# Kernel tuning notes

Measured on AMD Instinct MI355X. Metric: run time of the kernel, lower is better.

Reference implementation:

```python
import jax, jax.numpy as jnp
import numpy as np

B, H, P, L = 8, 512, 512, 2048
HIGH_STAB, LOW_STAB = 0.9, 0.99  # 0 <= high < |lambda| <= low <= 1 (discrete dynamics)


def setup_inputs() -> dict:
    key = jax.random.key(0)
    k_u, k_mag, k_ph, k_b, k_c, k_d = jax.random.split(key, 6)
    u = jax.random.normal(k_u, (B, H, L), dtype=jnp.float32)
    # Frozen diagonal reservoir state matrix Lambda_bar: complex eigenvalues with
    # magnitude in (high_stability, low_stability], random phase (stored as real/imag pairs).
    mag = jax.random.uniform(k_mag, (P,), minval=HIGH_STAB, maxval=LOW_STAB)
    phase = jax.random.uniform(k_ph, (P,), minval=0.0, maxval=2.0 * np.pi)
    Lambda_bar_ri = jnp.stack([mag * jnp.cos(phase), mag * jnp.sin(phase)], axis=-1)  # (P,2)
    B_bar_ri = jax.random.normal(k_b, (P, H, 2), dtype=jnp.float32)  # complex B_bar as real pairs
    C_ri = jax.random.normal(k_c, (H, P, 2), dtype=jnp.float32)      # complex C as real pairs
    D = jax.random.normal(k_d, (H, H), dtype=jnp.float32)
    return {"u": u, "Lambda_bar_ri": Lambda_bar_ri, "B_bar_ri": B_bar_ri, "C_ri": C_ri, "D": D}


def _binary_op(e_i, e_j):
    A_i, Bu_i = e_i
    A_j, Bu_j = e_j
    return (A_j * A_i, A_j * Bu_i + Bu_j)


def reference(u, Lambda_bar_ri, B_bar_ri, C_ri, D):
    Lam = jax.lax.complex(Lambda_bar_ri[:, 0], Lambda_bar_ri[:, 1])        # (P,)
    B_bar = jax.lax.complex(B_bar_ri[..., 0], B_bar_ri[..., 1])            # (P,H)
    C = jax.lax.complex(C_ri[..., 0], C_ri[..., 1])                        # (H,P)
    # Bu_t = B_bar @ u_t for all t, batched: (B,P,L) complex
    Bu = jnp.einsum('ph,bhl->bpl', B_bar, u.astype(B_bar.dtype))
    A = jnp.broadcast_to(Lam[None, :, None], Bu.shape)                     # (B,P,L)
    # Parallel associative scan: x_t = Lam * x_{t-1} + Bu_t
    _, x = jax.lax.associative_scan(_binary_op, (A, Bu), axis=2)           # (B,P,L)
    C_A_Bu = jnp.einsum('hp,bpl->bhl', C, x).real                          # (B,H,L)
    # torch.einsum('hh,bhl->bhl', D, u) uses only the diagonal of D
    Du = jnp.diagonal(D)[None, :, None] * u
    return jax.nn.gelu(C_A_Bu + Du, approximate=False)
```

## Files before the change

kernel.cpp:

```cpp
#include <hip/hip_runtime.h>
#include <cstdint>
#include <cstddef>

#define BB 8
#define HH 512
#define PP 512
#define LL 2048

typedef __attribute__((ext_vector_type(8))) __bf16 bf16x8;
typedef __attribute__((ext_vector_type(4))) float f32x4;

__device__ __forceinline__ uint16_t f2bf(float f) {
  uint32_t u = __builtin_bit_cast(uint32_t, f);
  u += 0x7FFFu + ((u >> 16) & 1u);
  return (uint16_t)(u >> 16);
}

__device__ __forceinline__ void async_copy16(const void* gptr, void* ldsptr) {
  __builtin_amdgcn_global_load_lds(
      (const __attribute__((address_space(1))) unsigned int*)gptr,
      (__attribute__((address_space(3))) unsigned int*)ldsptr,
      16, 0, 0);
}

__global__ __launch_bounds__(256) void prep_mats(
    const float* __restrict__ Bbar, const float* __restrict__ Cri,
    const float* __restrict__ Dm,
    uint16_t* __restrict__ A1, uint16_t* __restrict__ A2,
    float* __restrict__ Dd) {
  int idx = blockIdx.x * 256 + threadIdx.x;
  int p = idx >> 9, h = idx & 511;
  A1[(size_t)p * 512 + h]          = f2bf(Bbar[((size_t)p * 512 + h) * 2 + 0]);
  A1[(size_t)(512 + p) * 512 + h]  = f2bf(Bbar[((size_t)p * 512 + h) * 2 + 1]);
  int h2 = idx >> 9, p2 = idx & 511;
  A2[(size_t)h2 * 1024 + p2]        = f2bf( Cri[((size_t)h2 * 512 + p2) * 2 + 0]);
  A2[(size_t)h2 * 1024 + 512 + p2]  = f2bf(-Cri[((size_t)h2 * 512 + p2) * 2 + 1]);
  if (idx < 512) Dd[idx] = Dm[(size_t)idx * 512 + idx];
}

__global__ __launch_bounds__(256) void scan_kernel(
    const float* __restrict__ Lam, uint16_t* __restrict__ Bu) {
  const int gt = blockIdx.x * 256 + threadIdx.x;
  const int wave = gt >> 6, lane = gt & 63;
  const int b = wave >> 9, p = wave & 511;
  const float lr = Lam[p * 2 + 0], li = Lam[p * 2 + 1];
  float ar = lr, ai = li;
#pragma unroll
  for (int s = 0; s < 5; ++s) { float nr = ar * ar - ai * ai, ni = 2.f * ar * ai; ar = nr; ai = ni; }

  uint16_t* rowre = Bu + ((size_t)(b * 1024 + p)) * 2048 + lane * 32;
  uint16_t* rowim = Bu + ((size_t)(b * 1024 + 512 + p)) * 2048 + lane * 32;
  uint4 vr[4], vi[4];
#pragma unroll
  for (int q = 0; q < 4; ++q) { vr[q] = ((const uint4*)rowre)[q]; vi[q] = ((const uint4*)rowim)[q]; }

  float xr[32], xi[32];
  float sr = 0.f, si = 0.f;
#pragma unroll
  for (int q = 0; q < 4; ++q) {
    uint32_t wr[4] = {vr[q].x, vr[q].y, vr[q].z, vr[q].w};
    uint32_t wi[4] = {vi[q].x, vi[q].y, vi[q].z, vi[q].w};
#pragma unroll
    for (int d = 0; d < 4; ++d) {
      float br0 = __builtin_bit_cast(float, wr[d] << 16);
      float bi0 = __builtin_bit_cast(float, wi[d] << 16);
      float br1 = __builtin_bit_cast(float, wr[d] & 0xFFFF0000u);
      float bi1 = __builtin_bit_cast(float, wi[d] & 0xFFFF0000u);
      int j = q * 8 + d * 2;
      float nr = lr * sr - li * si + br0, ni = lr * si + li * sr + bi0;
      sr = nr; si = ni; xr[j] = sr; xi[j] = si;
      nr = lr * sr - li * si + br1; ni = lr * si + li * sr + bi1;
      sr = nr; si = ni; xr[j + 1] = sr; xi[j + 1] = si;
    }
  }
  float Ar = ar, Ai = ai, Sr = sr, Si = si;
#pragma unroll
  for (int off = 1; off < 64; off <<= 1) {
    float pAr = __shfl_up(Ar, off), pAi = __shfl_up(Ai, off);
    float pSr = __shfl_up(Sr, off), pSi = __shfl_up(Si, off);
    if (lane >= off) {
      float tSr = Ar * pSr - Ai * pSi + Sr;
      float tSi = Ar * pSi + Ai * pSr + Si;
      float tAr = Ar * pAr - Ai * pAi;
      float tAi = Ar * pAi + Ai * pAr;
      Sr = tSr; Si = tSi; Ar = tAr; Ai = tAi;
    }
  }
  float Cr = __shfl_up(Sr, 1), Ci = __shfl_up(Si, 1);
  if (lane == 0) { Cr = 0.f; Ci = 0.f; }
  float fr_ = lr * Cr - li * Ci, fi_ = lr * Ci + li * Cr;
#pragma unroll
  for (int j = 0; j < 32; ++j) {
    xr[j] += fr_; xi[j] += fi_;
    float nfr = fr_ * lr - fi_ * li, nfi = fr_ * li + fi_ * lr;
    fr_ = nfr; fi_ = nfi;
  }
#pragma unroll
  for (int q = 0; q < 4; ++q) {
    uint32_t wr[4], wi[4];
#pragma unroll
    for (int d = 0; d < 4; ++d) {
      int j = q * 8 + d * 2;
      wr[d] = (uint32_t)f2bf(xr[j]) | ((uint32_t)f2bf(xr[j + 1]) << 16);
      wi[d] = (uint32_t)f2bf(xi[j]) | ((uint32_t)f2bf(xi[j + 1]) << 16);
    }
    ((uint4*)rowre)[q] = make_uint4(wr[0], wr[1], wr[2], wr[3]);
    ((uint4*)rowim)[q] = make_uint4(wi[0], wi[1], wi[2], wi[3]);
  }
}

__global__ __launch_bounds__(256) void gemm1_fused(
    const uint16_t* __restrict__ A, const float* __restrict__ U,
    uint16_t* __restrict__ Bu) {
  __shared__ __align__(16) uint16_t Alds[2][128 * 32];
  __shared__ __align__(16) uint16_t Blds[2][128 * 40];
  const int t = threadIdx.x, lane = t & 63, w = t >> 6;
  const int m0 = blockIdx.y * 128, n0 = blockIdx.x * 128, b = blockIdx.z;

  const int ra = t >> 2;
  const int qa = ((t & 3) ^ ((ra >> 1) & 3)) * 8;
  const uint16_t* gA0 = A + (size_t)(m0 + ra) * 512 + qa;
  const uint16_t* gA1 = A + (size_t)(m0 + 64 + ra) * 512 + qa;

  const int kp = t >> 4, lg = t & 15;
  const float* gB = U + ((size_t)b * 512 + 2 * kp) * 2048 + n0 + lg * 8;
  const int bcol = ((kp >> 2) ^ (lg & 3)) * 8 + (kp & 3) * 2;

  f32x4 acc[4][4];
#pragma unroll
  for (int i = 0; i < 4; ++i)
#pragma unroll
    for (int j = 0; j < 4; ++j) acc[i][j] = (f32x4){0.f, 0.f, 0.f, 0.f};

  const int wm = (w >> 1) * 64, wn = (w & 1) * 64;
  const int fr = lane & 15, fq = lane >> 4;
  const int aswz = (fq ^ ((fr >> 1) & 3)) * 8;

  float4 pb0, pb1, pb2, pb3;
  async_copy16(gA0, &Alds[0][t * 8]);
  async_copy16(gA1, &Alds[0][2048 + t * 8]);
  pb0 = *(const float4*)(gB);
  pb1 = *(const float4*)(gB + 4);
  pb2 = *(const float4*)(gB + 2048);
  pb3 = *(const float4*)(gB + 2052);
  {
    float r0[8] = {pb0.x, pb0.y, pb0.z, pb0.w, pb1.x, pb1.y, pb1.z, pb1.w};
    float r1[8] = {pb2.x, pb2.y, pb2.z, pb2.w, pb3.x, pb3.y, pb3.z, pb3.w};
#pragma unroll
    for (int j = 0; j < 8; ++j)
      *(uint32_t*)&Blds[0][(lg * 8 + j) * 40 + bcol] =
          (uint32_t)f2bf(r0[j]) | ((uint32_t)f2bf(r1[j]) << 16);
  }
  __syncthreads();

#pragma unroll 2
  for (int it = 0; it < 16; ++it) {
    const int cur = it & 1, nxt = cur ^ 1;
    const bool pre = (it < 15);
    if (pre) {
      const int kb = (it + 1) * 32;
      async_copy16(gA0 + kb, &Alds[nxt][t * 8]);
      async_copy16(gA1 + kb, &Alds[nxt][2048 + t * 8]);
      const float* s0 = gB + (size_t)kb * 2048;
      pb0 = *(const float4*)(s0);
      pb1 = *(const float4*)(s0 + 4);
      pb2 = *(const float4*)(s0 + 2048);
      pb3 = *(const float4*)(s0 + 2052);
    }
    bf16x8 af[4], bfr[4];
#pragma unroll
    for (int i = 0; i < 4; ++i)
      af[i] = *(const bf16x8*)&Alds[cur][(wm + i * 16 + fr) * 32 + aswz];
#pragma unroll
    for (int j = 0; j < 4; ++j) {
      int n = wn + j * 16 + fr;
      bfr[j] = *(const bf16x8*)&Blds[cur][n * 40 + ((fq ^ ((n >> 3) & 3)) * 8)];
    }
#pragma unroll
    for (int i = 0; i < 4; ++i)
#pragma unroll
      for (int j = 0; j < 4; ++j)
        acc[i][j] = __builtin_amdgcn_mfma_f32_16x16x32_bf16(af[i], bfr[j], acc[i][j], 0, 0, 0);
    if (pre) {
      float r0[8] = {pb0.x, pb0.y, pb0.z, pb0.w, pb1.x, pb1.y, pb1.z, pb1.w};
      float r1[8] = {pb2.x, pb2.y, pb2.z, pb2.w, pb3.x, pb3.y, pb3.z, pb3.w};
#pragma unroll
      for (int j = 0; j < 8; ++j)
        *(uint32_t*)&Blds[nxt][(lg * 8 + j) * 40 + bcol] =
            (uint32_t)f2bf(r0[j]) | ((uint32_t)f2bf(r1[j]) << 16);
      __syncthreads();
    }
  }

  uint16_t* O = Bu + ((size_t)b * 1024 + m0) * 2048 + n0;
#pragma unroll
  for (int i = 0; i < 4; ++i)
#pragma unroll
    for (int j = 0; j < 4; ++j)
#pragma unroll
      for (int r = 0; r < 4; ++r) {
        int mm = wm + i * 16 + fq * 4 + r;
        int nn = wn + j * 16 + fr;
        O[(size_t)mm * 2048 + nn] = f2bf(acc[i][j][r]);
      }
}

__global__ __launch_bounds__(256) void gemm2_fused(
    const uint16_t* __restrict__ A, const uint16_t* __restrict__ X,
    float* __restrict__ Out, const float* __restrict__ Dd,
    const float* __restrict__ Uu) {
  __shared__ __align__(16) uint16_t Alds[2][128 * 32];
  __shared__ __align__(16) uint16_t Blds[2][128 * 40];
  const int t = threadIdx.x, lane = t & 63, w = t >> 6;
  const int m0 = blockIdx.y * 128, n0 = blockIdx.x * 128, b = blockIdx.z;

  const int ra = t >> 2;
  const int qa = ((t & 3) ^ ((ra >> 1) & 3)) * 8;
  const uint16_t* gA0 = A + (size_t)(m0 + ra) * 1024 + qa;
  const uint16_t* gA1 = A + (size_t)(m0 + 64 + ra) * 1024 + qa;

  const int kp = t >> 4, lg = t & 15;
  const uint16_t* gB = X + ((size_t)b * 1024 + 2 * kp) * 2048 + n0 + lg * 8;
  const int bcol = ((kp >> 2) ^ (lg & 3)) * 8 + (kp & 3) * 2;

  f32x4 acc[4][4];
#pragma unroll
  for (int i = 0; i < 4; ++i)
#pragma unroll
    for (int j = 0; j < 4; ++j) acc[i][j] = (f32x4){0.f, 0.f, 0.f, 0.f};

  const int wm = (w >> 1) * 64, wn = (w & 1) * 64;
  const int fr = lane & 15, fq = lane >> 4;
  const int aswz = (fq ^ ((fr >> 1) & 3)) * 8;

  uint4 q0, q1;
  async_copy16(gA0, &Alds[0][t * 8]);
  async_copy16(gA1, &Alds[0][2048 + t * 8]);
  q0 = *(const uint4*)(gB);
  q1 = *(const uint4*)(gB + 2048);
  {
    uint32_t u0[4] = {q0.x, q0.y, q0.z, q0.w};
    uint32_t u1[4] = {q1.x, q1.y, q1.z, q1.w};
#pragma unroll
    for (int d = 0; d < 4; ++d) {
      *(uint32_t*)&Blds[0][(lg * 8 + 2 * d + 0) * 40 + bcol] = (u0[d] & 0xFFFFu) | (u1[d] << 16);
      *(uint32_t*)&Blds[0][(lg * 8 + 2 * d + 1) * 40 + bcol] = (u0[d] >> 16) | (u1[d] & 0xFFFF0000u);
    }
  }
  __syncthreads();

#pragma unroll 2
  for (int it = 0; it < 32; ++it) {
    const int cur = it & 1, nxt = cur ^ 1;
    const bool pre = (it < 31);
    if (pre) {
      const int kb = (it + 1) * 32;
      async_copy16(gA0 + kb, &Alds[nxt][t * 8]);
      async_copy16(gA1 + kb, &Alds[nxt][2048 + t * 8]);
      const uint16_t* s0 = gB + (size_t)kb * 2048;
      q0 = *(const uint4*)(s0);
      q1 = *(const uint4*)(s0 + 2048);
    }
    bf16x8 af[4], bfr[4];
#pragma unroll
    for (int i = 0; i < 4; ++i)
      af[i] = *(const bf16x8*)&Alds[cur][(wm + i * 16 + fr) * 32 + aswz];
#pragma unroll
    for (int j = 0; j < 4; ++j) {
      int n = wn + j * 16 + fr;
      bfr[j] = *(const bf16x8*)&Blds[cur][n * 40 + ((fq ^ ((n >> 3) & 3)) * 8)];
    }
#pragma unroll
    for (int i = 0; i < 4; ++i)
#pragma unroll
      for (int j = 0; j < 4; ++j)
        acc[i][j] = __builtin_amdgcn_mfma_f32_16x16x32_bf16(af[i], bfr[j], acc[i][j], 0, 0, 0);
    if (pre) {
      uint32_t u0[4] = {q0.x, q0.y, q0.z, q0.w};
      uint32_t u1[4] = {q1.x, q1.y, q1.z, q1.w};
#pragma unroll
      for (int d = 0; d < 4; ++d) {
        *(uint32_t*)&Blds[nxt][(lg * 8 + 2 * d + 0) * 40 + bcol] = (u0[d] & 0xFFFFu) | (u1[d] << 16);
        *(uint32_t*)&Blds[nxt][(lg * 8 + 2 * d + 1) * 40 + bcol] = (u0[d] >> 16) | (u1[d] & 0xFFFF0000u);
      }
      __syncthreads();
    }
  }

  const size_t base = ((size_t)b * 512 + m0) * 2048 + n0;
  float* O = Out + base;
  const float* Ub = Uu + base;
#pragma unroll
  for (int i = 0; i < 4; ++i)
#pragma unroll
    for (int r = 0; r < 4; ++r) {
      int mm = wm + i * 16 + fq * 4 + r;
      float dv = Dd[m0 + mm];
#pragma unroll
      for (int j = 0; j < 4; ++j) {
        int nn = wn + j * 16 + fr;
        float xv = acc[i][j][r] + dv * Ub[(size_t)mm * 2048 + nn];
        O[(size_t)mm * 2048 + nn] = 0.5f * xv * (1.f + erff(xv * 0.70710678118654752f));
      }
    }
}

extern "C" void kernel_launch(void* const* d_in, const int* in_sizes, int n_in,
                              void* d_out, int out_size, void* d_ws, size_t ws_size,
                              hipStream_t stream) {
  const float* u    = (const float*)d_in[0];
  const float* Lam  = (const float*)d_in[1];
  const float* Bbar = (const float*)d_in[2];
  const float* Cri  = (const float*)d_in[3];
  const float* Dm   = (const float*)d_in[4];
  float* out = (float*)d_out;

  char* ws = (char*)d_ws;
  uint16_t* Bu = (uint16_t*)(ws);
  uint16_t* A1 = (uint16_t*)(ws + 33554432);
  uint16_t* A2 = (uint16_t*)(ws + 34603008);
  float*    Dd = (float*)   (ws + 35651584);

  prep_mats<<<1024, 256, 0, stream>>>(Bbar, Cri, Dm, A1, A2, Dd);
  gemm1_fused<<<dim3(16, 8, BB), 256, 0, stream>>>(A1, u, Bu);
  scan_kernel<<<1024, 256, 0, stream>>>(Lam, Bu);
  gemm2_fused<<<dim3(16, 4, BB), 256, 0, stream>>>(A2, Bu, out, Dd, u);
}
```

Baseline: 193.0 us.

## Load GEMM A fragments directly to registers and double K-step per iteration

Both GEMM kernels stop staging the weight matrix A through LDS via global_load_lds. Each wave now reads its MFMA A fragments straight from global memory into registers, double-buffered. The K step per loop iteration goes from 32 to 64, with two B sub-tiles in LDS and one barrier per 64 of K, which halves the synchronisation count. The cost is more VGPR pressure and redundant global loads of A across the waves that share rows, which rely on cache hits.

```diff
diff --git a/kernel.cpp b/kernel.cpp
--- a/kernel.cpp
+++ b/kernel.cpp
@@ -14,13 +14,6 @@
   uint32_t u = __builtin_bit_cast(uint32_t, f);
   u += 0x7FFFu + ((u >> 16) & 1u);
   return (uint16_t)(u >> 16);
-}
-
-__device__ __forceinline__ void async_copy16(const void* gptr, void* ldsptr) {
-  __builtin_amdgcn_global_load_lds(
-      (const __attribute__((address_space(1))) unsigned int*)gptr,
-      (__attribute__((address_space(3))) unsigned int*)ldsptr,
-      16, 0, 0);
 }
 
 __global__ __launch_bounds__(256) void prep_mats(
@@ -112,44 +105,169 @@
 __global__ __launch_bounds__(256) void gemm1_fused(
     const uint16_t* __restrict__ A, const float* __restrict__ U,
     uint16_t* __restrict__ Bu) {
-  __shared__ __align__(16) uint16_t Alds[2][128 * 32];
-  __shared__ __align__(16) uint16_t Blds[2][128 * 40];
+  __shared__ __align__(16) uint16_t Blds[2][2][128 * 40];
   const int t = threadIdx.x, lane = t & 63, w = t >> 6;
   const int m0 = blockIdx.y * 128, n0 = blockIdx.x * 128, b = blockIdx.z;
-
-  const int ra = t >> 2;
-  const int qa = ((t & 3) ^ ((ra >> 1) & 3)) * 8;
-  const uint16_t* gA0 = A + (size_t)(m0 + ra) * 512 + qa;
-  const uint16_t* gA1 = A + (size_t)(m0 + 64 + ra) * 512 + qa;
 
   const int kp = t >> 4, lg = t & 15;
   const float* gB = U + ((size_t)b * 512 + 2 * kp) * 2048 + n0 + lg * 8;
   const int bcol = ((kp >> 2) ^ (lg & 3)) * 8 + (kp & 3) * 2;
 
-  f32x4 acc[4][4];
-#pragma unroll
-  for (int i = 0; i < 4; ++i)
-#pragma unroll
-    for (int j = 0; j < 4; ++j) acc[i][j] = (f32x4){0.f, 0.f, 0.f, 0.f};
-
   const int wm = (w >> 1) * 64, wn = (w & 1) * 64;
   const int fr = lane & 15, fq = lane >> 4;
-  const int aswz = (fq ^ ((fr >> 1) & 3)) * 8;
-
-  float4 pb0, pb1, pb2, pb3;
-  async_copy16(gA0, &Alds[0][t * 8]);
-  async_copy16(gA1, &Alds[0][2048 + t * 8]);
-  pb0 = *(const float4*)(gB);
-  pb1 = *(const float4*)(gB + 4);
-  pb2 = *(const float4*)(gB + 2048);
-  pb3 = *(const float4*)(gB + 2052);
-  {
-    float r0[8] = {pb0.x, pb0.y, pb0.z, pb0.w, pb1.x, pb1.y, pb1.z, pb1.w};
-    float r1[8] = {pb2.x, pb2.y, pb2.z, pb2.w, pb3.x, pb3.y, pb3.z, pb3.w};
+  const uint16_t* gA = A + (size_t)(m0 + wm + fr) * 512 + fq * 8;
+
+  f32x4 acc[4][4];
+#pragma unroll
+  for (int i = 0; i < 4; ++i)
+#pragma unroll
+    for (int j = 0; j < 4; ++j) acc[i][j] = (f32x4){0.f, 0.f, 0.f, 0.f};
+
+  bf16x8 afA[2][4], afB[2][4];
+  float4 p0[2], p1[2], p2[2], p3[2];
+
+#pragma unroll
+  for (int s = 0; s < 2; ++s) {
+    const float* sp = gB + (size_t)(32 * s) * 2048;
+    p0[s] = *(const float4*)(sp);
+    p1[s] = *(const float4*)(sp + 4);
+    p2[s] = *(const float4*)(sp + 2048);
+    p3[s] = *(const float4*)(sp + 2052);
+  }
+#pragma unroll
+  for (int i = 0; i < 4; ++i) {
+    afA[0][i] = *(const bf16x8*)(gA + (size_t)i * 16 * 512);
+    afB[0][i] = *(const bf16x8*)(gA + (size_t)i * 16 * 512 + 32);
+  }
+#pragma unroll
+  for (int s = 0; s < 2; ++s) {
+    float r0[8] = {p0[s].x, p0[s].y, p0[s].z, p0[s].w, p1[s].x, p1[s].y, p1[s].z, p1[s].w};
+    float r1[8] = {p2[s].x, p2[s].y, p2[s].z, p2[s].w, p3[s].x, p3[s].y, p3[s].z, p3[s].w};
 #pragma unroll
     for (int j = 0; j < 8; ++j)
-      *(uint32_t*)&Blds[0][(lg * 8 + j) * 40 + bcol] =
+      *(uint32_t*)&Blds[0][s][(lg * 8 + j) * 40 + bcol] =
           (uint32_t)f2bf(r0[j]) | ((uint32_t)f2bf(r1[j]) << 16);
+  }
+  __syncthreads();
+
+#pragma unroll 2
+  for (int it = 0; it < 8; ++it) {
+    const int cur = it & 1, nxt = cur ^ 1;
+    const bool pre = (it < 7);
+    const int kn = (it + 1) * 64;
+    if (pre) {
+#pragma unroll
+      for (int s = 0; s < 2; ++s) {
+        const float* sp = gB + (size_t)(kn + 32 * s) * 2048;
+        p0[s] = *(const float4*)(sp);
+        p1[s] = *(const float4*)(sp + 4);
+        p2[s] = *(const float4*)(sp + 2048);
+        p3[s] = *(const float4*)(sp + 2052);
+      }
+#pragma unroll
+      for (int i = 0; i < 4; ++i) {
+        afA[nxt][i] = *(const bf16x8*)(gA + (size_t)i * 16 * 512 + kn);
+        afB[nxt][i] = *(const bf16x8*)(gA + (size_t)i * 16 * 512 + kn + 32);
+      }
+    }
+    bf16x8 bfr[4];
+#pragma unroll
+    for (int j = 0; j < 4; ++j) {
+      int n = wn + j * 16 + fr;
+      bfr[j] = *(const bf16x8*)&Blds[cur][0][n * 40 + ((fq ^ ((n >> 3) & 3)) * 8)];
+    }
+#pragma unroll
+    for (int i = 0; i < 4; ++i)
+#pragma unroll
+      for (int j = 0; j < 4; ++j)
+        acc[i][j] = __builtin_amdgcn_mfma_f32_16x16x32_bf16(afA[cur][i], bfr[j], acc[i][j], 0, 0, 0);
+    if (pre) {
+      float r0[8] = {p0[0].x, p0[0].y, p0[0].z, p0[0].w, p1[0].x, p1[0].y, p1[0].z, p1[0].w};
+      float r1[8] = {p2[0].x, p2[0].y, p2[0].z, p2[0].w, p3[0].x, p3[0].y, p3[0].z, p3[0].w};
+#pragma unroll
+      for (int j = 0; j < 8; ++j)
+        *(uint32_t*)&Blds[nxt][0][(lg * 8 + j) * 40 + bcol] =
+            (uint32_t)f2bf(r0[j]) | ((uint32_t)f2bf(r1[j]) << 16);
+    }
+#pragma unroll
+    for (int j = 0; j < 4; ++j) {
+      int n = wn + j * 16 + fr;
+      bfr[j] = *(const bf16x8*)&Blds[cur][1][n * 40 + ((fq ^ ((n >> 3) & 3)) * 8)];
+    }
+#pragma unroll
+    for (int i = 0; i < 4; ++i)
+#pragma unroll
+      for (int j = 0; j < 4; ++j)
+        acc[i][j] = __builtin_amdgcn_mfma_f32_16x16x32_bf16(afB[cur][i], bfr[j], acc[i][j], 0, 0, 0);
+    if (pre) {
+      float r0[8] = {p0[1].x, p0[1].y, p0[1].z, p0[1].w, p1[1].x, p1[1].y, p1[1].z, p1[1].w};
+      float r1[8] = {p2[1].x, p2[1].y, p2[1].z, p2[1].w, p3[1].x, p3[1].y, p3[1].z, p3[1].w};
+#pragma unroll
+      for (int j = 0; j < 8; ++j)
+        *(uint32_t*)&Blds[nxt][1][(lg * 8 + j) * 40 + bcol] =
+            (uint32_t)f2bf(r0[j]) | ((uint32_t)f2bf(r1[j]) << 16);
+      __syncthreads();
+    }
+  }
+
+  uint16_t* O = Bu + ((size_t)b * 1024 + m0) * 2048 + n0;
+#pragma unroll
+  for (int i = 0; i < 4; ++i)
+#pragma unroll
+    for (int j = 0; j < 4; ++j)
+#pragma unroll
+      for (int r = 0; r < 4; ++r) {
+        int mm = wm + i * 16 + fq * 4 + r;
+        int nn = wn + j * 16 + fr;
+        O[(size_t)mm * 2048 + nn] = f2bf(acc[i][j][r]);
+      }
+}
+
+__global__ __launch_bounds__(256) void gemm2_fused(
+    const uint16_t* __restrict__ A, const uint16_t* __restrict__ X,
+    float* __restrict__ Out, const float* __restrict__ Dd,
+    const float* __restrict__ Uu) {
+  __shared__ __align__(16) uint16_t Blds[2][2][128 * 40];
+  const int t = threadIdx.x, lane = t & 63, w = t >> 6;
+  const int m0 = blockIdx.y * 128, n0 = blockIdx.x * 128, b = blockIdx.z;
+
+  const int kp = t >> 4, lg = t & 15;
+  const uint16_t* gB = X + ((size_t)b * 1024 + 2 * kp) * 2048 + n0 + lg * 8;
+  const int bcol = ((kp >> 2) ^ (lg & 3)) * 8 + (kp & 3) * 2;
+
+  const int wm = (w >> 1) * 64, wn = (w & 1) * 64;
+  const int fr = lane & 15, fq = lane >> 4;
+  const uint16_t* gA = A + (size_t)(m0 + wm + fr) * 1024 + fq * 8;
+
+  f32x4 acc[4][4];
+#pragma unroll
+  for (int i = 0; i < 4; ++i)
+#pragma unroll
+    for (int j = 0; j < 4; ++j) acc[i][j] = (f32x4){0.f, 0.f, 0.f, 0.f};
+
+  bf16x8 afA[2][4], afB[2][4];
+  uint4 q0[2], q1[2];
+
+#pragma unroll
+  for (int s = 0; s < 2; ++s) {
+    const uint16_t* sp = gB + (size_t)(32 * s) * 2048;
+    q0[s] = *(const uint4*)(sp);
+    q1[s] = *(const uint4*)(sp + 2048);
+  }
+#pragma unroll
+  for (int i = 0; i < 4; ++i) {
+    afA[0][i] = *(const bf16x8*)(gA + (size_t)i * 16 * 1024);
+    afB[0][i] = *(const bf16x8*)(gA + (size_t)i * 16 * 1024 + 32);
+  }
+#pragma unroll
+  for (int s = 0; s < 2; ++s) {
+    uint32_t u0[4] = {q0[s].x, q0[s].y, q0[s].z, q0[s].w};
+    uint32_t u1[4] = {q1[s].x, q1[s].y, q1[s].z, q1[s].w};
+#pragma unroll
+    for (int d = 0; d < 4; ++d) {
+      *(uint32_t*)&Blds[0][s][(lg * 8 + 2 * d + 0) * 40 + bcol] = (u0[d] & 0xFFFFu) | (u1[d] << 16);
+      *(uint32_t*)&Blds[0][s][(lg * 8 + 2 * d + 1) * 40 + bcol] = (u0[d] >> 16) | (u1[d] & 0xFFFF0000u);
+    }
   }
   __syncthreads();
 
@@ -157,131 +275,57 @@
   for (int it = 0; it < 16; ++it) {
     const int cur = it & 1, nxt = cur ^ 1;
     const bool pre = (it < 15);
-    if (pre) {
-      const int kb = (it + 1) * 32;
-      async_copy16(gA0 + kb, &Alds[nxt][t * 8]);
-      async_copy16(gA1 + kb, &Alds[nxt][2048 + t * 8]);
-      const float* s0 = gB + (size_t)kb * 2048;
-      pb0 = *(const float4*)(s0);
-      pb1 = *(const float4*)(s0 + 4);
-      pb2 = *(const float4*)(s0 + 2048);
-      pb3 = *(const float4*)(s0 + 2052);
-    }
-    bf16x8 af[4], bfr[4];
-#pragma unroll
-    for (int i = 0; i < 4; ++i)
-      af[i] = *(const bf16x8*)&Alds[cur][(wm + i * 16 + fr) * 32 + aswz];
+    const int kn = (it + 1) * 64;
+    if (pre) {
+#pragma unroll
+      for (int s = 0; s < 2; ++s) {
+        const uint16_t* sp = gB + (size_t)(kn + 32 * s) * 2048;
+        q0[s] = *(const uint4*)(sp);
+        q1[s] = *(const uint4*)(sp + 2048);
+      }
+#pragma unroll
+      for (int i = 0; i < 4; ++i) {
+        afA[nxt][i] = *(const bf16x8*)(gA + (size_t)i * 16 * 1024 + kn);
+        afB[nxt][i] = *(const bf16x8*)(gA + (size_t)i * 16 * 1024 + kn + 32);
+      }
+    }
+    bf16x8 bfr[4];
 #pragma unroll
     for (int j = 0; j < 4; ++j) {
       int n = wn + j * 16 + fr;
-      bfr[j] = *(const bf16x8*)&Blds[cur][n * 40 + ((fq ^ ((n >> 3) & 3)) * 8)];
+      bfr[j] = *(const bf16x8*)&Blds[cur][0][n * 40 + ((fq ^ ((n >> 3) & 3)) * 8)];
     }
 #pragma unroll
     for (int i = 0; i < 4; ++i)
 #pragma unroll
       for (int j = 0; j < 4; ++j)
-        acc[i][j] = __builtin_amdgcn_mfma_f32_16x16x32_bf16(af[i], bfr[j], acc[i][j], 0, 0, 0);
-    if (pre) {
-      float r0[8] = {pb0.x, pb0.y, pb0.z, pb0.w, pb1.x, pb1.y, pb1.z, pb1.w};
-      float r1[8] = {pb2.x, pb2.y, pb2.z, pb2.w, pb3.x, pb3.y, pb3.z, pb3.w};
-#pragma unroll
-      for (int j = 0; j < 8; ++j)
-        *(uint32_t*)&Blds[nxt][(lg * 8 + j) * 40 + bcol] =
-            (uint32_t)f2bf(r0[j]) | ((uint32_t)f2bf(r1[j]) << 16);
-      __syncthreads();
-    }
-  }
-
-  uint16_t* O = Bu + ((size_t)b * 1024 + m0) * 2048 + n0;
-#pragma unroll
-  for (int i = 0; i < 4; ++i)
-#pragma unroll
-    for (int j = 0; j < 4; ++j)
-#pragma unroll
-      for (int r = 0; r < 4; ++r) {
-        int mm = wm + i * 16 + fq * 4 + r;
-        int nn = wn + j * 16 + fr;
-        O[(size_t)mm * 2048 + nn] = f2bf(acc[i][j][r]);
-      }
-}
-
-__global__ __launch_bounds__(256) void gemm2_fused(
-    const uint16_t* __restrict__ A, const uint16_t* __restrict__ X,
-    float* __restrict__ Out, const float* __restrict__ Dd,
-    const float* __restrict__ Uu) {
-  __shared__ __align__(16) uint16_t Alds[2][128 * 32];
-  __shared__ __align__(16) uint16_t Blds[2][128 * 40];
-  const int t = threadIdx.x, lane = t & 63, w = t >> 6;
-  const int m0 = blockIdx.y * 128, n0 = blockIdx.x * 128, b = blockIdx.z;
-
-  const int ra = t >> 2;
-  const int qa = ((t & 3) ^ ((ra >> 1) & 3)) * 8;
-  const uint16_t* gA0 = A + (size_t)(m0 + ra) * 1024 + qa;
-  const uint16_t* gA1 = A + (size_t)(m0 + 64 + ra) * 1024 + qa;
-
-  const int kp = t >> 4, lg = t & 15;
-  const uint16_t* gB = X + ((size_t)b * 1024 + 2 * kp) * 2048 + n0 + lg * 8;
-  const int bcol = ((kp >> 2) ^ (lg & 3)) * 8 + (kp & 3) * 2;
-
-  f32x4 acc[4][4];
-#pragma unroll
-  for (int i = 0; i < 4; ++i)
-#pragma unroll
-    for (int j = 0; j < 4; ++j) acc[i][j] = (f32x4){0.f, 0.f, 0.f, 0.f};
-
-  const int wm = (w >> 1) * 64, wn = (w & 1) * 64;
-  const int fr = lane & 15, fq = lane >> 4;
-  const int aswz = (fq ^ ((fr >> 1) & 3)) * 8;
-
-  uint4 q0, q1;
-  async_copy16(gA0, &Alds[0][t * 8]);
-  async_copy16(gA1, &Alds[0][2048 + t * 8]);
-  q0 = *(const uint4*)(gB);
-  q1 = *(const uint4*)(gB + 2048);
-  {
-    uint32_t u0[4] = {q0.x, q0.y, q0.z, q0.w};
-    uint32_t u1[4] = {q1.x, q1.y, q1.z, q1.w};
-#pragma unroll
-    for (int d = 0; d < 4; ++d) {
-      *(uint32_t*)&Blds[0][(lg * 8 + 2 * d + 0) * 40 + bcol] = (u0[d] & 0xFFFFu) | (u1[d] << 16);
-      *(uint32_t*)&Blds[0][(lg * 8 + 2 * d + 1) * 40 + bcol] = (u0[d] >> 16) | (u1[d] & 0xFFFF0000u);
-    }
-  }
-  __syncthreads();
-
-#pragma unroll 2
-  for (int it = 0; it < 32; ++it) {
-    const int cur = it & 1, nxt = cur ^ 1;
-    const bool pre = (it < 31);
-    if (pre) {
-      const int kb = (it + 1) * 32;
-      async_copy16(gA0 + kb, &Alds[nxt][t * 8]);
-      async_copy16(gA1 + kb, &Alds[nxt][2048 + t * 8]);
-      const uint16_t* s0 = gB + (size_t)kb * 2048;
-      q0 = *(const uint4*)(s0);
-      q1 = *(const uint4*)(s0 + 2048);
-    }
-    bf16x8 af[4], bfr[4];
-#pragma unroll
-    for (int i = 0; i < 4; ++i)
-      af[i] = *(const bf16x8*)&Alds[cur][(wm + i * 16 + fr) * 32 + aswz];
+        acc[i][j] = __builtin_amdgcn_mfma_f32_16x16x32_bf16(afA[cur][i], bfr[j], acc[i][j], 0, 0, 0);
+    if (pre) {
+      uint32_t u0[4] = {q0[0].x, q0[0].y, q0[0].z, q0[0].w};
+      uint32_t u1[4] = {q1[0].x, q1[0].y, q1[0].z, q1[0].w};
+#pragma unroll
+      for (int d = 0; d < 4; ++d) {
+        *(uint32_t*)&Blds[nxt][0][(lg * 8 + 2 * d + 0) * 40 + bcol] = (u0[d] & 0xFFFFu) | (u1[d] << 16);
+        *(uint32_t*)&Blds[nxt][0][(lg * 8 + 2 * d + 1) * 40 + bcol] = (u0[d] >> 16) | (u1[d] & 0xFFFF0000u);
+      }
+    }
 #pragma unroll
     for (int j = 0; j < 4; ++j) {
       int n = wn + j * 16 + fr;
-      bfr[j] = *(const bf16x8*)&Blds[cur][n * 40 + ((fq ^ ((n >> 3) & 3)) * 8)];
+      bfr[j] = *(const bf16x8*)&Blds[cur][1][n * 40 + ((fq ^ ((n >> 3) & 3)) * 8)];
     }
 #pragma unroll
     for (int i = 0; i < 4; ++i)
 #pragma unroll
       for (int j = 0; j < 4; ++j)
-        acc[i][j] = __builtin_amdgcn_mfma_f32_16x16x32_bf16(af[i], bfr[j], acc[i][j], 0, 0, 0);
-    if (pre) {
-      uint32_t u0[4] = {q0.x, q0.y, q0.z, q0.w};
-      uint32_t u1[4] = {q1.x, q1.y, q1.z, q1.w};
+        acc[i][j] = __builtin_amdgcn_mfma_f32_16x16x32_bf16(afB[cur][i], bfr[j], acc[i][j], 0, 0, 0);
+    if (pre) {
+      uint32_t u0[4] = {q0[1].x, q0[1].y, q0[1].z, q0[1].w};
+      uint32_t u1[4] = {q1[1].x, q1[1].y, q1[1].z, q1[1].w};
 #pragma unroll
       for (int d = 0; d < 4; ++d) {
-        *(uint32_t*)&Blds[nxt][(lg * 8 + 2 * d + 0) * 40 + bcol] = (u0[d] & 0xFFFFu) | (u1[d] << 16);
-        *(uint32_t*)&Blds[nxt][(lg * 8 + 2 * d + 1) * 40 + bcol] = (u0[d] >> 16) | (u1[d] & 0xFFFF0000u);
+        *(uint32_t*)&Blds[nxt][1][(lg * 8 + 2 * d + 0) * 40 + bcol] = (u0[d] & 0xFFFFu) | (u1[d] << 16);
+        *(uint32_t*)&Blds[nxt][1][(lg * 8 + 2 * d + 1) * 40 + bcol] = (u0[d] >> 16) | (u1[d] & 0xFFFF0000u);
       }
       __syncthreads();
     }
```

Measured after the change: 207.7 us. +7.6%, slower.
